# Optimization experiments

Hardware: AMD Instinct MI355X
Metric: run time of the kernel (lower is better)

The kernel has to match this reference:

```python
import jax, jax.numpy as jnp
import numpy as np

NUM_CLUSTERS = 64
DIM = 256
EPS = 1e-12  # torch F.normalize eps


def setup_inputs() -> dict:
    key = jax.random.key(0)
    k1, k2, k3, k4 = jax.random.split(key, 4)
    x = jax.random.normal(k1, (128, DIM, 32, 32), dtype=jnp.float32)
    # nn.Conv2d(256, K, 1) params: weight (K, C, 1, 1) -> store as (K, C); bias (K,)
    fan_in = DIM
    bound = 1.0 / np.sqrt(fan_in)
    conv_w = jax.random.uniform(k2, (NUM_CLUSTERS, DIM), jnp.float32, -bound, bound)
    conv_b = jax.random.uniform(k3, (NUM_CLUSTERS,), jnp.float32, -bound, bound)
    centroids = jax.random.uniform(k4, (NUM_CLUSTERS, DIM), jnp.float32)  # torch.rand
    return {"x": x, "conv_w": conv_w, "conv_b": conv_b, "centroids": centroids}


def _l2norm(v, axis):
    n = jnp.sqrt(jnp.sum(v * v, axis=axis, keepdims=True))
    return v / jnp.maximum(n, EPS)


def reference(x, conv_w, conv_b, centroids):
    N, C, H, W = x.shape
    K = conv_w.shape[0]
    # L2-normalize over channel dim
    x = _l2norm(x, axis=1)                      # (N, C, H, W)
    xf = x.reshape(N, C, H * W)                 # (N, C, P)
    # 1x1 conv == per-pixel linear over channels
    logits = jnp.einsum('ncp,kc->nkp', xf, conv_w) + conv_b[None, :, None]
    a = jax.nn.softmax(logits, axis=1)          # (N, K, P) softmax over clusters
    # VLAD via matmul decomposition: sum_p a[n,k,p]*(x[n,:,p] - c[k,:])
    agg = jnp.einsum('nkp,ncp->nkc', a, xf)     # (N, K, C)
    asum = jnp.sum(a, axis=-1)                  # (N, K)
    vlad = agg - asum[:, :, None] * centroids[None, :, :]
    vlad = _l2norm(vlad, axis=2)                # intra-normalization
    vlad = vlad.reshape(N, K * C)
    return _l2norm(vlad, axis=1)
```

## Files before the change

### kernel.cpp

```cpp
#include <hip/hip_runtime.h>
#include <math.h>


#define EPSF 1e-12f

typedef __attribute__((ext_vector_type(8))) __bf16 bf16x8;
typedef __attribute__((ext_vector_type(4))) float f32x4;
typedef __attribute__((ext_vector_type(4))) unsigned int u32x4;

#define MFMA(a, b, c) __builtin_amdgcn_mfma_f32_16x16x32_bf16((a), (b), (c), 0, 0, 0)

__device__ __forceinline__ bf16x8 as_bf(u32x4 v) { return __builtin_bit_cast(bf16x8, v); }

__device__ __forceinline__ unsigned packsplit(float x) {
    const unsigned u  = __float_as_uint(x);
    const unsigned hi = u & 0xFFFF0000u;
    const float lof   = x - __uint_as_float(hi);
    return hi | (__float_as_uint(lof) >> 16);
}

struct u32pair { unsigned h, l; };

__device__ __forceinline__ u32pair splitpair(float f0, float f1) {
    const unsigned u0 = __float_as_uint(f0), u1 = __float_as_uint(f1);
    u32pair r;
    r.h = __builtin_amdgcn_perm(u1, u0, 0x07060302u);
    const float l0 = f0 - __uint_as_float(u0 & 0xFFFF0000u);
    const float l1 = f1 - __uint_as_float(u1 & 0xFFFF0000u);
    r.l = __builtin_amdgcn_perm(__float_as_uint(l1), __float_as_uint(l0), 0x07060302u);
    return r;
}

__device__ __forceinline__ void unpack2q(const u32x4 q0, const u32x4 q1,
                                         u32x4& hi, u32x4& lo) {
    hi[0] = __builtin_amdgcn_perm(q0[1], q0[0], 0x07060302u);
    lo[0] = __builtin_amdgcn_perm(q0[1], q0[0], 0x05040100u);
    hi[1] = __builtin_amdgcn_perm(q0[3], q0[2], 0x07060302u);
    lo[1] = __builtin_amdgcn_perm(q0[3], q0[2], 0x05040100u);
    hi[2] = __builtin_amdgcn_perm(q1[1], q1[0], 0x07060302u);
    lo[2] = __builtin_amdgcn_perm(q1[1], q1[0], 0x05040100u);
    hi[3] = __builtin_amdgcn_perm(q1[3], q1[2], 0x07060302u);
    lo[3] = __builtin_amdgcn_perm(q1[3], q1[2], 0x05040100u);
}

__device__ __forceinline__ void split8v(const float* xv, u32x4& hi, u32x4& lo) {
    #pragma unroll
    for (int w2 = 0; w2 < 4; ++w2) {
        const u32pair r = splitpair(xv[2*w2], xv[2*w2+1]);
        hi[w2] = r.h;
        lo[w2] = r.l;
    }
}

__global__ void split_w_kernel(const float* __restrict__ wmat,
                               unsigned* __restrict__ whiG,
                               unsigned* __restrict__ wloG) {
    const int idx = blockIdx.x * 256 + threadIdx.x;
    const int mt = idx >> 9, s = (idx >> 6) & 7, l = idx & 63;
    const int k = mt * 16 + (l & 15);
    const int cb = s * 32 + 8 * (l >> 4);
    const float* wr = wmat + k * 256 + cb;
    const float4 f0 = *(const float4*)wr;
    const float4 f1 = *(const float4*)(wr + 4);
    const float xv[8] = {f0.x, f0.y, f0.z, f0.w, f1.x, f1.y, f1.z, f1.w};
    u32x4 hi, lo; split8v(xv, hi, lo);
    *(u32x4*)(whiG + idx * 4) = hi;
    *(u32x4*)(wloG + idx * 4) = lo;
}

__global__ __launch_bounds__(256, 4) void netvlad_p1(
    const float* __restrict__ x,
    const unsigned* __restrict__ whiG, const unsigned* __restrict__ wloG,
    const float* __restrict__ bias, unsigned* __restrict__ aG,
    float* __restrict__ asum_part) {

    __shared__ __align__(16) unsigned xs1[2][4096];
    __shared__ float asum_lds[4][64];
    const int t = threadIdx.x;
    const int w = t >> 6, l = t & 63;
    const int l15 = l & 15, lg4 = l >> 4;
    const int n = blockIdx.x & 127, e = blockIdx.x >> 7;
    const size_t ximg = (size_t)n * 256 * 1024;
    const int p0 = e * 128;
    const int cs = lg4 * 8;

    const float* src1[4];
    unsigned dst1[4];
    #pragma unroll
    for (int i = 0; i < 4; ++i) {
        const int rr = (w * 4 + i) * 2 + (l >> 5);
        const int psrc = ((l & 31) * 4) ^ (((rr >> 3) & 1) << 4);
        src1[i] = x + ximg + (size_t)rr * 1024 + p0 + psrc;
        dst1[i] = (unsigned)((w * 4 + i) * 256);
    }
    #define P1DMA(s_, b_) { _Pragma("unroll")                                 \
        for (int i = 0; i < 4; ++i)                                           \
            __builtin_amdgcn_global_load_lds(                                 \
                (const __attribute__((address_space(1))) void*)(src1[i] + (size_t)(s_) * 32768), \
                (__attribute__((address_space(3))) void*)(&xs1[b_][dst1[i]]), \
                16, 0, 0); }

    f32x4 acc1[4][2];
    #pragma unroll
    for (int i = 0; i < 4; ++i) {
        acc1[i][0] = f32x4{0.f, 0.f, 0.f, 0.f};
        acc1[i][1] = f32x4{0.f, 0.f, 0.f, 0.f};
    }
    float ssa[2] = {0.f, 0.f};
    const int swzf = (lg4 & 1) << 4;

    P1DMA(0, 0);
    u32x4 wh[4], wl[4];
    #pragma unroll
    for (int s = 0; s < 8; ++s) {
        __syncthreads();
        if (s < 7) P1DMA(s + 1, (s + 1) & 1);
        #pragma unroll
        for (int mt = 0; mt < 4; ++mt) {
            const int fo = ((mt * 8 + s) * 64 + l) * 4;
            wh[mt] = *(const u32x4*)(whiG + fo);
            wl[mt] = *(const u32x4*)(wloG + fo);
        }
        const unsigned* xb = xs1[s & 1];
        #pragma unroll
        for (int ntl = 0; ntl < 2; ++ntl) {
            const int colr = (((2 * w + ntl) * 16 + l15) ^ swzf);
            float xv[8];
            #pragma unroll
            for (int j = 0; j < 8; ++j)
                xv[j] = __uint_as_float(xb[(cs + j) * 128 + colr]);
            #pragma unroll
            for (int j = 0; j < 8; ++j) ssa[ntl] = fmaf(xv[j], xv[j], ssa[ntl]);
            u32x4 bhi, blo; split8v(xv, bhi, blo);
            #pragma unroll
            for (int mt = 0; mt < 4; ++mt) {
                acc1[mt][ntl] = MFMA(as_bf(wh[mt]), as_bf(bhi), acc1[mt][ntl]);
                acc1[mt][ntl] = MFMA(as_bf(wh[mt]), as_bf(blo), acc1[mt][ntl]);
                acc1[mt][ntl] = MFMA(as_bf(wl[mt]), as_bf(bhi), acc1[mt][ntl]);
            }
        }
    }
    #pragma unroll
    for (int ntl = 0; ntl < 2; ++ntl) {
        ssa[ntl] += __shfl_xor(ssa[ntl], 16);
        ssa[ntl] += __shfl_xor(ssa[ntl], 32);
    }

    f32x4 biasv[4];
    #pragma unroll
    for (int mt = 0; mt < 4; ++mt)
        biasv[mt] = *(const f32x4*)(bias + mt * 16 + 4 * lg4);

    float asum_loc[16];
    #pragma unroll
    for (int i = 0; i < 16; ++i) asum_loc[i] = 0.f;

    #pragma unroll
    for (int ntl = 0; ntl < 2; ++ntl) {
        const int p = p0 + (2 * w + ntl) * 16 + l15;
        const float rn = 1.f / fmaxf(sqrtf(ssa[ntl]), EPSF);
        float lgv[16];
        #pragma unroll
        for (int mt = 0; mt < 4; ++mt)
            #pragma unroll
            for (int r = 0; r < 4; ++r)
                lgv[mt * 4 + r] = fmaf(acc1[mt][ntl][r], rn, biasv[mt][r]);
        float mx = lgv[0];
        #pragma unroll
        for (int i = 1; i < 16; ++i) mx = fmaxf(mx, lgv[i]);
        mx = fmaxf(mx, __shfl_xor(mx, 16));
        mx = fmaxf(mx, __shfl_xor(mx, 32));
        float den = 0.f;
        #pragma unroll
        for (int i = 0; i < 16; ++i) { lgv[i] = __expf(lgv[i] - mx); den += lgv[i]; }
        den += __shfl_xor(den, 16);
        den += __shfl_xor(den, 32);
        const float inv = 1.f / den;
        #pragma unroll
        for (int mt = 0; mt < 4; ++mt)
            #pragma unroll
            for (int r = 0; r < 4; ++r) {
                const float av = lgv[mt * 4 + r] * inv;
                asum_loc[mt * 4 + r] += av;
                aG[((size_t)n * 64 + mt * 16 + 4 * lg4 + r) * 1024 + p] =
                    packsplit(av * rn);
            }
    }

    #pragma unroll
    for (int i = 0; i < 16; ++i) {
        float s = asum_loc[i];
        s += __shfl_xor(s, 1);
        s += __shfl_xor(s, 2);
        s += __shfl_xor(s, 4);
        s += __shfl_xor(s, 8);
        if (l15 == 0) asum_lds[w][(i >> 2) * 16 + 4 * lg4 + (i & 3)] = s;
    }
    __syncthreads();
    if (t < 64)
        asum_part[((size_t)n * 8 + e) * 64 + t] =
            asum_lds[0][t] + asum_lds[1][t] + asum_lds[2][t] + asum_lds[3][t];
}

__global__ __launch_bounds__(256, 4) void netvlad_p2(
    const float* __restrict__ x, const unsigned* __restrict__ aG,
    float* __restrict__ out0, float* __restrict__ out1) {

    __shared__ __align__(16) unsigned xs[2][2048];
    __shared__ __align__(16) unsigned as2[2][2048];

    const int t = threadIdx.x;
    const int w = t >> 6, l = t & 63;
    const int l15 = l & 15, lg4 = l >> 4;
    const int n = blockIdx.x & 127;
    const int z = blockIdx.x >> 7;
    const int cq = z & 3, ph = z >> 2;
    const size_t ximg = (size_t)n * 256 * 1024;
    const int c0 = cq * 64;
    const int pb0 = ph * 512;

    const float* srcx[2];
    const unsigned* srca[2];
    unsigned ldsq[2];
    #pragma unroll
    for (int i = 0; i < 2; ++i) {
        const int Q = w * 128 + i * 64 + l;
        const int row = Q >> 3, q = Q & 7;
        const int qs = q ^ (row & 7);
        srcx[i] = x + ximg + (size_t)(c0 + row) * 1024 + pb0 + qs * 4;
        srca[i] = aG + ((size_t)n * 64 + row) * 1024 + pb0 + qs * 4;
        ldsq[i] = (unsigned)((w * 128 + i * 64) * 4);
    }

    #define P2DMA(s_, b_) { _Pragma("unroll")                                 \
        for (int i = 0; i < 2; ++i) {                                         \
            __builtin_amdgcn_global_load_lds(                                 \
                (const __attribute__((address_space(1))) void*)(srcx[i] + (s_) * 32), \
                (__attribute__((address_space(3))) void*)(&xs[b_][ldsq[i]]),  \
                16, 0, 0);                                                    \
            __builtin_amdgcn_global_load_lds(                                 \
                (const __attribute__((address_space(1))) void*)(srca[i] + (s_) * 32), \
                (__attribute__((address_space(3))) void*)(&as2[b_][ldsq[i]]), \
                16, 0, 0);                                                    \
        } }

    f32x4 acc[4];
    #pragma unroll
    for (int mt = 0; mt < 4; ++mt) acc[mt] = f32x4{0.f, 0.f, 0.f, 0.f};

    const int sA = (((lg4 * 2)     ^ (l15 & 7)) << 2);
    const int sB = (((lg4 * 2 + 1) ^ (l15 & 7)) << 2);
    const int rx = w * 16 + l15;

    P2DMA(0, 0);
    #pragma unroll
    for (int ks = 0; ks < 16; ++ks) {
        __syncthreads();
        if (ks < 15) P2DMA(ks + 1, (ks + 1) & 1);
        const unsigned* xb = xs[ks & 1];
        const unsigned* ab = as2[ks & 1];

        const u32x4 fx0 = *(const u32x4*)(xb + rx * 32 + sA);
        const u32x4 fx1 = *(const u32x4*)(xb + rx * 32 + sB);
        float xv[8];
        xv[0] = __uint_as_float(fx0[0]); xv[1] = __uint_as_float(fx0[1]);
        xv[2] = __uint_as_float(fx0[2]); xv[3] = __uint_as_float(fx0[3]);
        xv[4] = __uint_as_float(fx1[0]); xv[5] = __uint_as_float(fx1[1]);
        xv[6] = __uint_as_float(fx1[2]); xv[7] = __uint_as_float(fx1[3]);
        u32x4 bhi, blo; split8v(xv, bhi, blo);

        #pragma unroll
        for (int mt = 0; mt < 4; ++mt) {
            const int ra = mt * 16 + l15;
            const u32x4 pa  = *(const u32x4*)(ab + ra * 32 + sA);
            const u32x4 pbq = *(const u32x4*)(ab + ra * 32 + sB);
            u32x4 ahi, alo; unpack2q(pa, pbq, ahi, alo);
            acc[mt] = MFMA(as_bf(ahi), as_bf(bhi), acc[mt]);
            acc[mt] = MFMA(as_bf(ahi), as_bf(blo), acc[mt]);
            acc[mt] = MFMA(as_bf(alo), as_bf(bhi), acc[mt]);
        }
    }

    float* op = (ph ? out1 : out0) + (size_t)n * 16384;
    #pragma unroll
    for (int mt = 0; mt < 4; ++mt)
        #pragma unroll
        for (int r = 0; r < 4; ++r)
            op[(mt * 16 + 4 * lg4 + r) * 256 + c0 + w * 16 + l15] = acc[mt][r];
}

__global__ __launch_bounds__(256) void netvlad_epi(
    float* __restrict__ out, const float* __restrict__ out1,
    const float* __restrict__ asum_part, const float* __restrict__ cent) {
    __shared__ float wred[4];
    __shared__ float gs_sh;
    const int n = blockIdx.x;
    const int t = threadIdx.x;
    const int k = t >> 2;
    const int q = t & 3;
    float* op = out + (size_t)n * 16384 + k * 256 + q * 64;
    const float* o1 = out1 + (size_t)n * 16384 + k * 256 + q * 64;
    const float* cp = cent + k * 256 + q * 64;
    float as = 0.f;
    #pragma unroll
    for (int e2 = 0; e2 < 8; ++e2)
        as += asum_part[((size_t)n * 8 + e2) * 64 + k];

    float v[64];
    float ss = 0.f;
    #pragma unroll
    for (int i = 0; i < 64; i += 4) {
        const float4 a0 = *(const float4*)&op[i];
        const float4 a1 = *(const float4*)&o1[i];
        const float4 cv = *(const float4*)&cp[i];
        v[i+0] = fmaf(-as, cv.x, a0.x + a1.x);
        v[i+1] = fmaf(-as, cv.y, a0.y + a1.y);
        v[i+2] = fmaf(-as, cv.z, a0.z + a1.z);
        v[i+3] = fmaf(-as, cv.w, a0.w + a1.w);
        ss = fmaf(v[i+0], v[i+0], ss);
        ss = fmaf(v[i+1], v[i+1], ss);
        ss = fmaf(v[i+2], v[i+2], ss);
        ss = fmaf(v[i+3], v[i+3], ss);
    }
    ss += __shfl_xor(ss, 1);
    ss += __shfl_xor(ss, 2);
    const float iscale = 1.f / fmaxf(sqrtf(ss), EPSF);

    float gsum = (q == 0) ? ss * iscale * iscale : 0.f;
    #pragma unroll
    for (int off = 4; off < 64; off <<= 1) gsum += __shfl_xor(gsum, off);
    if ((t & 63) == 0) wred[t >> 6] = gsum;
    __syncthreads();
    if (t == 0) {
        const float tot = wred[0] + wred[1] + wred[2] + wred[3];
        gs_sh = 1.f / fmaxf(sqrtf(tot), EPSF);
    }
    __syncthreads();
    const float fs = iscale * gs_sh;
    #pragma unroll
    for (int i = 0; i < 64; i += 4) {
        float4 w4;
        w4.x = v[i+0] * fs; w4.y = v[i+1] * fs;
        w4.z = v[i+2] * fs; w4.w = v[i+3] * fs;
        *(float4*)&op[i] = w4;
    }
}

extern "C" void kernel_launch(void* const* d_in, const int* in_sizes, int n_in,
                              void* d_out, int out_size, void* d_ws, size_t ws_size,
                              hipStream_t stream) {
    (void)in_sizes; (void)n_in; (void)out_size; (void)ws_size;
    const float* x    = (const float*)d_in[0];
    const float* wmat = (const float*)d_in[1];
    const float* b    = (const float*)d_in[2];
    const float* cent = (const float*)d_in[3];
    float* out = (float*)d_out;
    unsigned* whiG = (unsigned*)d_ws;
    unsigned* wloG = whiG + 8192;
    float* asum_part = (float*)(whiG + 16384);
    unsigned* aG   = whiG + 16384 + 65536;
    float* out1    = (float*)(aG + 8388608);

    split_w_kernel<<<8, 256, 0, stream>>>(wmat, whiG, wloG);
    netvlad_p1<<<1024, 256, 0, stream>>>(x, whiG, wloG, b, aG, asum_part);
    netvlad_p2<<<1024, 256, 0, stream>>>(x, aG, out, out1);
    netvlad_epi<<<128, 256, 0, stream>>>(out, out1, asum_part, cent);
}
```

Baseline: 81.92 us.

## Halve phase-1 LDS staging tile and raise occupancy bound to eight blocks

The phase-1 kernel now stages 64-pixel halves of each 32-channel slab instead of 128 pixels, halving the double-buffered LDS footprint and doubling the pipeline stage count to 16. The launch bound goes from 4 to 8 blocks per SM, to allow more resident waves and hide load latency. Weight fragments are reloaded only on even stages. The cost is twice as many barriers and DMA issues per block, and a tighter register budget that may cause spills.

```diff
diff --git a/kernel.cpp b/kernel.cpp
--- a/kernel.cpp
+++ b/kernel.cpp
@@ -68,13 +68,13 @@
     *(u32x4*)(wloG + idx * 4) = lo;
 }
 
-__global__ __launch_bounds__(256, 4) void netvlad_p1(
+__global__ __launch_bounds__(256, 8) void netvlad_p1(
     const float* __restrict__ x,
     const unsigned* __restrict__ whiG, const unsigned* __restrict__ wloG,
     const float* __restrict__ bias, unsigned* __restrict__ aG,
     float* __restrict__ asum_part) {
 
-    __shared__ __align__(16) unsigned xs1[2][4096];
+    __shared__ __align__(16) unsigned xs1[2][2048];
     __shared__ float asum_lds[4][64];
     const int t = threadIdx.x;
     const int w = t >> 6, l = t & 63;
@@ -84,19 +84,20 @@
     const int p0 = e * 128;
     const int cs = lg4 * 8;
 
-    const float* src1[4];
-    unsigned dst1[4];
-    #pragma unroll
-    for (int i = 0; i < 4; ++i) {
-        const int rr = (w * 4 + i) * 2 + (l >> 5);
-        const int psrc = ((l & 31) * 4) ^ (((rr >> 3) & 1) << 4);
-        src1[i] = x + ximg + (size_t)rr * 1024 + p0 + psrc;
-        dst1[i] = (unsigned)((w * 4 + i) * 256);
-    }
-    #define P1DMA(s_, b_) { _Pragma("unroll")                                 \
-        for (int i = 0; i < 4; ++i)                                           \
+    const float* src1[2];
+    unsigned dst1[2];
+    #pragma unroll
+    for (int i = 0; i < 2; ++i) {
+        const int rr = w * 8 + i * 4 + (l >> 4);
+        const int pc = ((l & 15) * 4) ^ (((rr >> 3) & 1) << 4);
+        src1[i] = x + ximg + (size_t)rr * 1024 + p0 + pc;
+        dst1[i] = (unsigned)((w * 8 + i * 4) * 64);
+    }
+    #define P1DMA(st_, b_) { _Pragma("unroll")                                \
+        for (int i = 0; i < 2; ++i)                                           \
             __builtin_amdgcn_global_load_lds(                                 \
-                (const __attribute__((address_space(1))) void*)(src1[i] + (size_t)(s_) * 32768), \
+                (const __attribute__((address_space(1))) void*)(src1[i]       \
+                    + (size_t)((st_) >> 1) * 32768 + ((st_) & 1) * 64),       \
                 (__attribute__((address_space(3))) void*)(&xs1[b_][dst1[i]]), \
                 16, 0, 0); }
 
@@ -112,38 +113,38 @@
     P1DMA(0, 0);
     u32x4 wh[4], wl[4];
     #pragma unroll
-    for (int s = 0; s < 8; ++s) {
+    for (int st = 0; st < 16; ++st) {
+        const int s = st >> 1, h = st & 1;
         __syncthreads();
-        if (s < 7) P1DMA(s + 1, (s + 1) & 1);
-        #pragma unroll
-        for (int mt = 0; mt < 4; ++mt) {
-            const int fo = ((mt * 8 + s) * 64 + l) * 4;
-            wh[mt] = *(const u32x4*)(whiG + fo);
-            wl[mt] = *(const u32x4*)(wloG + fo);
-        }
-        const unsigned* xb = xs1[s & 1];
-        #pragma unroll
-        for (int ntl = 0; ntl < 2; ++ntl) {
-            const int colr = (((2 * w + ntl) * 16 + l15) ^ swzf);
-            float xv[8];
-            #pragma unroll
-            for (int j = 0; j < 8; ++j)
-                xv[j] = __uint_as_float(xb[(cs + j) * 128 + colr]);
-            #pragma unroll
-            for (int j = 0; j < 8; ++j) ssa[ntl] = fmaf(xv[j], xv[j], ssa[ntl]);
-            u32x4 bhi, blo; split8v(xv, bhi, blo);
+        if (st < 15) P1DMA(st + 1, (st + 1) & 1);
+        if (h == 0) {
             #pragma unroll
             for (int mt = 0; mt < 4; ++mt) {
-                acc1[mt][ntl] = MFMA(as_bf(wh[mt]), as_bf(bhi), acc1[mt][ntl]);
-                acc1[mt][ntl] = MFMA(as_bf(wh[mt]), as_bf(blo), acc1[mt][ntl]);
-                acc1[mt][ntl] = MFMA(as_bf(wl[mt]), as_bf(bhi), acc1[mt][ntl]);
+                const int fo = ((mt * 8 + s) * 64 + l) * 4;
+                wh[mt] = *(const u32x4*)(whiG + fo);
+                wl[mt] = *(const u32x4*)(wloG + fo);
             }
         }
-    }
-    #pragma unroll
-    for (int ntl = 0; ntl < 2; ++ntl) {
-        ssa[ntl] += __shfl_xor(ssa[ntl], 16);
-        ssa[ntl] += __shfl_xor(ssa[ntl], 32);
+        const unsigned* xb = xs1[st & 1];
+        const int colr = (w * 16 + l15) ^ swzf;
+        float xv[8];
+        #pragma unroll
+        for (int j = 0; j < 8; ++j)
+            xv[j] = __uint_as_float(xb[(cs + j) * 64 + colr]);
+        #pragma unroll
+        for (int j = 0; j < 8; ++j) ssa[h] = fmaf(xv[j], xv[j], ssa[h]);
+        u32x4 bhi, blo; split8v(xv, bhi, blo);
+        #pragma unroll
+        for (int mt = 0; mt < 4; ++mt) {
+            acc1[mt][h] = MFMA(as_bf(wh[mt]), as_bf(bhi), acc1[mt][h]);
+            acc1[mt][h] = MFMA(as_bf(wh[mt]), as_bf(blo), acc1[mt][h]);
+            acc1[mt][h] = MFMA(as_bf(wl[mt]), as_bf(bhi), acc1[mt][h]);
+        }
+    }
+    #pragma unroll
+    for (int h = 0; h < 2; ++h) {
+        ssa[h] += __shfl_xor(ssa[h], 16);
+        ssa[h] += __shfl_xor(ssa[h], 32);
     }
 
     f32x4 biasv[4];
@@ -156,15 +157,15 @@
     for (int i = 0; i < 16; ++i) asum_loc[i] = 0.f;
 
     #pragma unroll
-    for (int ntl = 0; ntl < 2; ++ntl) {
-        const int p = p0 + (2 * w + ntl) * 16 + l15;
-        const float rn = 1.f / fmaxf(sqrtf(ssa[ntl]), EPSF);
+    for (int h = 0; h < 2; ++h) {
+        const int p = p0 + h * 64 + w * 16 + l15;
+        const float rn = 1.f / fmaxf(sqrtf(ssa[h]), EPSF);
         float lgv[16];
         #pragma unroll
         for (int mt = 0; mt < 4; ++mt)
             #pragma unroll
             for (int r = 0; r < 4; ++r)
-                lgv[mt * 4 + r] = fmaf(acc1[mt][ntl][r], rn, biasv[mt][r]);
+                lgv[mt * 4 + r] = fmaf(acc1[mt][h][r], rn, biasv[mt][r]);
         float mx = lgv[0];
         #pragma unroll
         for (int i = 1; i < 16; ++i) mx = fmaxf(mx, lgv[i]);
```

Measured after the change: 166.7 us. 104% more time.
